# Performance work log

Measured on AMD Instinct MI355X. Metric: run time of the kernel, lower is better.

The kernel has to match this reference:

```python
import jax, jax.numpy as jnp
import numpy as np
from jax import lax


def _maxpool_h(x):
    # MaxPool2d(kernel=(3,1), stride=(2,1), padding=(1,0)) on NCHW.
    # Torch pads with -inf for max pooling.
    return lax.reduce_window(
        x,
        -jnp.inf,
        lax.max,
        window_dimensions=(1, 1, 3, 1),
        window_strides=(1, 1, 2, 1),
        padding=((0, 0), (0, 0), (1, 1), (0, 0)),
    )


def setup_inputs() -> dict:
    key = jax.random.key(0)
    x = jax.random.normal(key, (32, 1, 8192, 256), dtype=jnp.float32)
    return {"x": x}


def reference(x) -> jnp.ndarray:
    out = _maxpool_h(x)  # [B, C, H', W]
    # Per-sample min-max normalization (vectorized over batch instead of the
    # original per-sample python loop).
    mx = jnp.max(out, axis=(1, 2, 3), keepdims=True)
    mn = jnp.min(out, axis=(1, 2, 3), keepdims=True)
    return (out - mn) / (mx - mn)
```

## Files before the change

kernel.cpp:

```cpp
#include <hip/hip_runtime.h>
#include <cfloat>

#define BATCH     32
#define H_IN      8192
#define H_OUT     4096
#define W         256
#define W4        64
#define CH        32
#define BLK_PER_B 32

__device__ __forceinline__ float4 max3_f4(float4 a, float4 b, float4 c) {
    float4 m;
    m.x = fmaxf(a.x, fmaxf(b.x, c.x));
    m.y = fmaxf(a.y, fmaxf(b.y, c.y));
    m.z = fmaxf(a.z, fmaxf(b.z, c.z));
    m.w = fmaxf(a.w, fmaxf(b.w, c.w));
    return m;
}

__global__ __launch_bounds__(256) void pool_partial(
        const float* __restrict__ x, float* __restrict__ out,
        float* __restrict__ partial_min, float* __restrict__ partial_max) {
    const int batch = blockIdx.x >> 5;
    const int blk   = blockIdx.x & 31;
    const int tid   = threadIdx.x;
    const int w4    = tid & 63;
    const int rg    = tid >> 6;
    const int h0    = blk * (BLK_PER_B * 4) + rg * CH;

    const float4* xin = (const float4*)x + (size_t)batch * H_IN * W4 + w4;
    float4*       po  = (float4*)out + ((size_t)batch * H_OUT + h0) * W4 + w4;

    float lmin = FLT_MAX, lmax = -FLT_MAX;

    float4 prev;
    const int r0 = 2 * h0 - 1;
    if (r0 >= 0) prev = xin[(size_t)r0 * W4];
    else         prev = make_float4(-FLT_MAX, -FLT_MAX, -FLT_MAX, -FLT_MAX);

    #pragma unroll 4
    for (int i = 0; i < CH; ++i) {
        const int r = 2 * (h0 + i);
        float4 a = xin[(size_t)r * W4];
        float4 c = xin[(size_t)(r + 1) * W4];
        float4 m = max3_f4(prev, a, c);
        po[(size_t)i * W4] = m;
        prev = c;
        lmax = fmaxf(lmax, fmaxf(fmaxf(m.x, m.y), fmaxf(m.z, m.w)));
        lmin = fminf(lmin, fminf(fminf(m.x, m.y), fminf(m.z, m.w)));
    }

    #pragma unroll
    for (int off = 32; off > 0; off >>= 1) {
        lmax = fmaxf(lmax, __shfl_down(lmax, off, 64));
        lmin = fminf(lmin, __shfl_down(lmin, off, 64));
    }
    __shared__ float smax[4], smin[4];
    const int lane = tid & 63;
    if (lane == 0) { smax[rg] = lmax; smin[rg] = lmin; }
    __syncthreads();
    if (tid == 0) {
        float bmax = smax[0], bmin = smin[0];
        #pragma unroll
        for (int i = 1; i < 4; ++i) {
            bmax = fmaxf(bmax, smax[i]);
            bmin = fminf(bmin, smin[i]);
        }
        partial_max[blockIdx.x] = bmax;
        partial_min[blockIdx.x] = bmin;
    }
}

__global__ void reduce_partials(const float* __restrict__ pmin,
                                const float* __restrict__ pmax,
                                float* __restrict__ stats) {
    const int b = blockIdx.x;
    const int t = threadIdx.x;
    float mn = (t < BLK_PER_B) ? pmin[b * BLK_PER_B + t] : FLT_MAX;
    float mx = (t < BLK_PER_B) ? pmax[b * BLK_PER_B + t] : -FLT_MAX;
    #pragma unroll
    for (int off = 16; off > 0; off >>= 1) {
        mn = fminf(mn, __shfl_down(mn, off, 64));
        mx = fmaxf(mx, __shfl_down(mx, off, 64));
    }
    if (t == 0) {
        stats[2 * b]     = mn;
        stats[2 * b + 1] = 1.0f / (mx - mn);
    }
}

__global__ __launch_bounds__(256) void normalize(float* __restrict__ out,
                                                 const float* __restrict__ stats) {
    const int b   = blockIdx.x >> 8;
    const int blk = blockIdx.x & 255;
    const float mn  = stats[2 * b];
    const float inv = stats[2 * b + 1];
    float4* p = (float4*)out + (size_t)b * (H_OUT * W4);
    const int base = blk * 1024 + threadIdx.x;
    #pragma unroll
    for (int i = 0; i < 4; ++i) {
        const int idx = base + i * 256;
        float4 v = p[idx];
        v.x = (v.x - mn) * inv;
        v.y = (v.y - mn) * inv;
        v.z = (v.z - mn) * inv;
        v.w = (v.w - mn) * inv;
        p[idx] = v;
    }
}

extern "C" void kernel_launch(void* const* d_in, const int* in_sizes, int n_in,
                              void* d_out, int out_size, void* d_ws, size_t ws_size,
                              hipStream_t stream) {
    const float* x   = (const float*)d_in[0];
    float*       out = (float*)d_out;
    float*       ws  = (float*)d_ws;

    float* pmin  = ws;
    float* pmax  = ws + 1024;
    float* stats = ws + 2048;

    pool_partial<<<BATCH * BLK_PER_B, 256, 0, stream>>>(x, out, pmin, pmax);
    reduce_partials<<<BATCH, 64, 0, stream>>>(pmin, pmax, stats);
    normalize<<<BATCH * 256, 256, 0, stream>>>(out, stats);
}
```

Measured before the change: 433.0 us.

## Recompute pooling in second pass and fuse normalization instead of storing intermediate

Splits the work into a min/max-only pooling pass and a second pass that recomputes the pooled values from the input, reduces per-batch stats in-block, and writes normalized output directly with nontemporal stores. This removes the intermediate write of pooled output, the read-modify-write normalize kernel, and one launch. In exchange the input is read twice.

```diff
diff --git a/kernel.cpp b/kernel.cpp
--- a/kernel.cpp
+++ b/kernel.cpp
@@ -4,10 +4,11 @@
 #define BATCH     32
 #define H_IN      8192
 #define H_OUT     4096
-#define W         256
 #define W4        64
 #define CH        32
 #define BLK_PER_B 32
+
+typedef float vfloat4 __attribute__((ext_vector_type(4)));
 
 __device__ __forceinline__ float4 max3_f4(float4 a, float4 b, float4 c) {
     float4 m;
@@ -18,18 +19,17 @@
     return m;
 }
 
-__global__ __launch_bounds__(256) void pool_partial(
-        const float* __restrict__ x, float* __restrict__ out,
+__global__ __launch_bounds__(256) void pool_minmax(
+        const float* __restrict__ x,
         float* __restrict__ partial_min, float* __restrict__ partial_max) {
     const int batch = blockIdx.x >> 5;
     const int blk   = blockIdx.x & 31;
     const int tid   = threadIdx.x;
     const int w4    = tid & 63;
     const int rg    = tid >> 6;
-    const int h0    = blk * (BLK_PER_B * 4) + rg * CH;
+    const int h0    = blk * 128 + rg * CH;
 
     const float4* xin = (const float4*)x + (size_t)batch * H_IN * W4 + w4;
-    float4*       po  = (float4*)out + ((size_t)batch * H_OUT + h0) * W4 + w4;
 
     float lmin = FLT_MAX, lmax = -FLT_MAX;
 
@@ -38,13 +38,12 @@
     if (r0 >= 0) prev = xin[(size_t)r0 * W4];
     else         prev = make_float4(-FLT_MAX, -FLT_MAX, -FLT_MAX, -FLT_MAX);
 
-    #pragma unroll 4
+    #pragma unroll 8
     for (int i = 0; i < CH; ++i) {
         const int r = 2 * (h0 + i);
         float4 a = xin[(size_t)r * W4];
         float4 c = xin[(size_t)(r + 1) * W4];
         float4 m = max3_f4(prev, a, c);
-        po[(size_t)i * W4] = m;
         prev = c;
         lmax = fmaxf(lmax, fmaxf(fmaxf(m.x, m.y), fmaxf(m.z, m.w)));
         lmin = fminf(lmin, fminf(fminf(m.x, m.y), fminf(m.z, m.w)));
@@ -56,8 +55,7 @@
         lmin = fminf(lmin, __shfl_down(lmin, off, 64));
     }
     __shared__ float smax[4], smin[4];
-    const int lane = tid & 63;
-    if (lane == 0) { smax[rg] = lmax; smin[rg] = lmin; }
+    if ((tid & 63) == 0) { smax[rg] = lmax; smin[rg] = lmin; }
     __syncthreads();
     if (tid == 0) {
         float bmax = smax[0], bmin = smin[0];
@@ -71,41 +69,53 @@
     }
 }
 
-__global__ void reduce_partials(const float* __restrict__ pmin,
-                                const float* __restrict__ pmax,
-                                float* __restrict__ stats) {
-    const int b = blockIdx.x;
-    const int t = threadIdx.x;
-    float mn = (t < BLK_PER_B) ? pmin[b * BLK_PER_B + t] : FLT_MAX;
-    float mx = (t < BLK_PER_B) ? pmax[b * BLK_PER_B + t] : -FLT_MAX;
-    #pragma unroll
-    for (int off = 16; off > 0; off >>= 1) {
-        mn = fminf(mn, __shfl_down(mn, off, 64));
-        mx = fmaxf(mx, __shfl_down(mx, off, 64));
+__global__ __launch_bounds__(256) void pool_norm(
+        const float* __restrict__ x,
+        const float* __restrict__ partial_min, const float* __restrict__ partial_max,
+        float* __restrict__ out) {
+    const int batch = blockIdx.x >> 5;
+    const int blk   = blockIdx.x & 31;
+    const int tid   = threadIdx.x;
+    const int w4    = tid & 63;
+    const int rg    = tid >> 6;
+    const int h0    = blk * 128 + rg * CH;
+
+    __shared__ float s_mn, s_inv;
+    if (tid < 64) {
+        float mn = (tid < BLK_PER_B) ? partial_min[batch * BLK_PER_B + tid] : FLT_MAX;
+        float mx = (tid < BLK_PER_B) ? partial_max[batch * BLK_PER_B + tid] : -FLT_MAX;
+        #pragma unroll
+        for (int off = 16; off > 0; off >>= 1) {
+            mn = fminf(mn, __shfl_down(mn, off, 64));
+            mx = fmaxf(mx, __shfl_down(mx, off, 64));
+        }
+        if (tid == 0) { s_mn = mn; s_inv = 1.0f / (mx - mn); }
     }
-    if (t == 0) {
-        stats[2 * b]     = mn;
-        stats[2 * b + 1] = 1.0f / (mx - mn);
-    }
-}
+    __syncthreads();
+    const float mn  = s_mn;
+    const float inv = s_inv;
 
-__global__ __launch_bounds__(256) void normalize(float* __restrict__ out,
-                                                 const float* __restrict__ stats) {
-    const int b   = blockIdx.x >> 8;
-    const int blk = blockIdx.x & 255;
-    const float mn  = stats[2 * b];
-    const float inv = stats[2 * b + 1];
-    float4* p = (float4*)out + (size_t)b * (H_OUT * W4);
-    const int base = blk * 1024 + threadIdx.x;
-    #pragma unroll
-    for (int i = 0; i < 4; ++i) {
-        const int idx = base + i * 256;
-        float4 v = p[idx];
-        v.x = (v.x - mn) * inv;
-        v.y = (v.y - mn) * inv;
-        v.z = (v.z - mn) * inv;
-        v.w = (v.w - mn) * inv;
-        p[idx] = v;
+    const float4* xin = (const float4*)x + (size_t)batch * H_IN * W4 + w4;
+    vfloat4*      po  = (vfloat4*)out + ((size_t)batch * H_OUT + h0) * W4 + w4;
+
+    float4 prev;
+    const int r0 = 2 * h0 - 1;
+    if (r0 >= 0) prev = xin[(size_t)r0 * W4];
+    else         prev = make_float4(-FLT_MAX, -FLT_MAX, -FLT_MAX, -FLT_MAX);
+
+    #pragma unroll 8
+    for (int i = 0; i < CH; ++i) {
+        const int r = 2 * (h0 + i);
+        float4 a = xin[(size_t)r * W4];
+        float4 c = xin[(size_t)(r + 1) * W4];
+        float4 m = max3_f4(prev, a, c);
+        prev = c;
+        vfloat4 v;
+        v.x = (m.x - mn) * inv;
+        v.y = (m.y - mn) * inv;
+        v.z = (m.z - mn) * inv;
+        v.w = (m.w - mn) * inv;
+        __builtin_nontemporal_store(v, po + (size_t)i * W4);
     }
 }
 
@@ -116,11 +126,9 @@
     float*       out = (float*)d_out;
     float*       ws  = (float*)d_ws;
 
-    float* pmin  = ws;
-    float* pmax  = ws + 1024;
-    float* stats = ws + 2048;
+    float* pmin = ws;
+    float* pmax = ws + 1024;
 
-    pool_partial<<<BATCH * BLK_PER_B, 256, 0, stream>>>(x, out, pmin, pmax);
-    reduce_partials<<<BATCH, 64, 0, stream>>>(pmin, pmax, stats);
-    normalize<<<BATCH * 256, 256, 0, stream>>>(out, stats);
+    pool_minmax<<<BATCH * BLK_PER_B, 256, 0, stream>>>(x, pmin, pmax);
+    pool_norm<<<BATCH * BLK_PER_B, 256, 0, stream>>>(x, pmin, pmax, out);
 }
```

Result: no change. 437.5 us (+1.0%).
